# Kernel optimization log

Hardware: AMD Instinct MI355X
Metric: run time of the kernel (lower is better)

The kernel has to match this reference:

```python
import jax, jax.numpy as jnp
import numpy as np

N_HEADS = 16
D_EMBED = 1024


def setup_inputs() -> dict:
    key = jax.random.key(0)
    k_x, k_win, k_bin, k_wout, k_bout = jax.random.split(key, 5)
    B, S, D = 4, 2048, D_EMBED
    # weights stored as (in, out) so y = x @ W + b (equivalent to torch Linear)
    x = jax.random.normal(k_x, (B, S, D), dtype=jnp.float32)
    W_in = jax.random.normal(k_win, (D, 3 * D), dtype=jnp.float32) * (D ** -0.5)
    b_in = jax.random.normal(k_bin, (3 * D,), dtype=jnp.float32) * 0.02
    W_out = jax.random.normal(k_wout, (D, D), dtype=jnp.float32) * (D ** -0.5)
    b_out = jax.random.normal(k_bout, (D,), dtype=jnp.float32) * 0.02
    return {"x": x, "W_in": W_in, "b_in": b_in, "W_out": W_out, "b_out": b_out,
            "causal_mask": 1}


def reference(x, W_in, b_in, W_out, b_out, causal_mask):
    B, S, D = x.shape
    H = N_HEADS
    dh = D // H
    qkv = x @ W_in + b_in                      # [B,S,3D]
    q, k, v = jnp.split(qkv, 3, axis=-1)
    q = q.reshape(B, S, H, dh)
    k = k.reshape(B, S, H, dh)
    v = v.reshape(B, S, H, dh)
    scores = jnp.einsum('bqhd,bkhd->bhqk', q, k)   # [B,H,S,S]
    if causal_mask:
        # original masks with -inf BEFORE scaling; -inf/sqrt(dh) == -inf
        tri = jnp.triu(jnp.ones((S, S), dtype=bool), k=1)
        scores = jnp.where(tri, -jnp.inf, scores)
    scores = scores / jnp.sqrt(jnp.asarray(dh, dtype=scores.dtype))
    attn = jax.nn.softmax(scores, axis=-1)
    out = jnp.einsum('bhqk,bkhd->bqhd', attn, v).reshape(B, S, D)
    return out @ W_out + b_out
```

## Files before the change

kernel.cpp:

```cpp
#include <hip/hip_runtime.h>
#include <hip/hip_bf16.h>
#include <stdint.h>
#include <string.h>

#define S_LEN 2048
#define NH    16
#define DH    64
#define D_EMB 1024
#define CSCALE 0.18033688011112042f

typedef __attribute__((ext_vector_type(8)))  short short8;
typedef __attribute__((ext_vector_type(4)))  float f32x4;
typedef __attribute__((ext_vector_type(16))) float f32x16;

__device__ __forceinline__ unsigned short f2bf(float f) {
  uint32_t u = __builtin_bit_cast(uint32_t, f);
  uint32_t r = (u + 0x7FFFu + ((u >> 16) & 1u)) >> 16;
  return (unsigned short)r;
}

__device__ __forceinline__ uint32_t pkbf(float a, float b) {
  float2 f; f.x = a; f.y = b;
  __hip_bfloat162 h = __float22bfloat162_rn(f);
  uint32_t r;
  memcpy(&r, &h, 4);
  return r;
}

__device__ __forceinline__ void gload16(const void* g, void* l) {
  __builtin_amdgcn_global_load_lds(
      (__attribute__((address_space(1))) void*)(g),
      (__attribute__((address_space(3))) void*)(l),
      16, 0, 0);
}

__device__ __forceinline__ f32x16 mfma32(short8 a, short8 b, f32x16 c) {
  return __builtin_amdgcn_mfma_f32_32x32x16_bf16(a, b, c, 0, 0, 0);
}


__global__ __launch_bounds__(256)
void cvt_bf16(const float* __restrict__ in, unsigned short* __restrict__ out, int n) {
  int i = (blockIdx.x * 256 + threadIdx.x) * 4;
  if (i >= n) return;
  float4 v = *(const float4*)&in[i];
  ushort4 o;
  o.x = f2bf(v.x); o.y = f2bf(v.y); o.z = f2bf(v.z); o.w = f2bf(v.w);
  *(ushort4*)&out[i] = o;
}

__global__ __launch_bounds__(256)
void transpose_cvt(const float* __restrict__ in, unsigned short* __restrict__ out,
                   int R, int C) {
  __shared__ float t[64][65];
  const int nbr = R >> 6;
  const int br = (blockIdx.x % nbr) << 6;
  const int bc = (blockIdx.x / nbr) << 6;
  const int tid = threadIdx.x;
  const int tr = tid >> 4;
  const int tc = (tid & 15) << 2;
#pragma unroll
  for (int i = 0; i < 4; ++i) {
    float4 v = *(const float4*)&in[(size_t)(br + tr + i * 16) * C + bc + tc];
    t[tr + i * 16][tc + 0] = v.x;
    t[tr + i * 16][tc + 1] = v.y;
    t[tr + i * 16][tc + 2] = v.z;
    t[tr + i * 16][tc + 3] = v.w;
  }
  __syncthreads();
#pragma unroll
  for (int i = 0; i < 4; ++i) {
    int c = tr + i * 16;
    ushort4 o;
    o.x = f2bf(t[tc + 0][c]);
    o.y = f2bf(t[tc + 1][c]);
    o.z = f2bf(t[tc + 2][c]);
    o.w = f2bf(t[tc + 3][c]);
    *(ushort4*)&out[(size_t)(bc + c) * R + br + tc] = o;
  }
}


template <int MODE>
__global__ __launch_bounds__(256, 2)
void gemm_bt(const unsigned short* __restrict__ A,
             const unsigned short* __restrict__ Bt,
             const float* __restrict__ bias,
             unsigned short* __restrict__ q_out,
             unsigned short* __restrict__ k_out,
             unsigned short* __restrict__ v_out,
             float* __restrict__ f_out,
             int M, int N, int K) {
  __shared__ __attribute__((aligned(16))) unsigned short As[2][128 * 64];
  __shared__ __attribute__((aligned(16))) unsigned short Bs[2][128 * 64];
  const int tid  = threadIdx.x;
  const int lane = tid & 63;
  const int w    = tid >> 6;
  const int grp  = lane >> 4;
  const int lc   = lane & 15;
  const int nbn  = N >> 7;
  const int bm   = blockIdx.x / nbn;
  const int bn   = blockIdx.x % nbn;
  const int wr   = w >> 1, wc = w & 1;

  f32x4 acc[4][4];
#pragma unroll
  for (int m = 0; m < 4; ++m)
#pragma unroll
    for (int n = 0; n < 4; ++n) acc[m][n] = f32x4{0.f, 0.f, 0.f, 0.f};

  const int srow = lane >> 3;
  const int scol = ((lane & 7) ^ srow) * 8;
  const int nkt  = K >> 6;

#define GSTAGE(buf_, kt_) do {                                               \
    _Pragma("unroll")                                                        \
    for (int c_ = 0; c_ < 4; ++c_) {                                         \
      const int rc_ = w * 32 + c_ * 8;                                       \
      gload16(&A[(size_t)(bm * 128 + rc_ + srow) * K + (kt_) * 64 + scol],   \
              (void*)(&As[buf_][rc_ * 64]));                                 \
      gload16(&Bt[(size_t)(bn * 128 + rc_ + srow) * K + (kt_) * 64 + scol],  \
              (void*)(&Bs[buf_][rc_ * 64]));                                 \
    }                                                                        \
  } while (0)

  GSTAGE(0, 0);
  __syncthreads();

  for (int kt = 0; kt < nkt; ++kt) {
    const int cur = kt & 1;
    if (kt + 1 < nkt) GSTAGE(cur ^ 1, kt + 1);
#pragma unroll
    for (int kk = 0; kk < 2; ++kk) {
      short8 af[4], bf[4];
#pragma unroll
      for (int m = 0; m < 4; ++m) {
        const int row = wr * 64 + m * 16 + lc;
        const int cb  = ((kk * 4 + grp) ^ (lc & 7)) * 8;
        af[m] = *(const short8*)(&As[cur][row * 64 + cb]);
      }
#pragma unroll
      for (int n = 0; n < 4; ++n) {
        const int row = wc * 64 + n * 16 + lc;
        const int cb  = ((kk * 4 + grp) ^ (lc & 7)) * 8;
        bf[n] = *(const short8*)(&Bs[cur][row * 64 + cb]);
      }
      __builtin_amdgcn_s_setprio(1);
#pragma unroll
      for (int m = 0; m < 4; ++m)
#pragma unroll
        for (int n = 0; n < 4; ++n)
          acc[m][n] = __builtin_amdgcn_mfma_f32_16x16x32_bf16(af[m], bf[n], acc[m][n], 0, 0, 0);
      __builtin_amdgcn_s_setprio(0);
    }
    __syncthreads();
  }
#undef GSTAGE

  const int gm0 = bm * 128 + wr * 64;
  const int gn0 = bn * 128 + wc * 64;
  if (MODE == 0) {
    const int seg = gn0 >> 10;
#pragma unroll
    for (int m = 0; m < 4; ++m) {
#pragma unroll
      for (int n = 0; n < 4; ++n) {
        const int gn = gn0 + n * 16 + lc;
        const float bv = bias[gn];
        const int j = gn & 1023;
        const int h = j >> 6, d = j & 63;
        const int gmb = gm0 + m * 16 + grp * 4;
        const int b = gmb >> 11;
        const size_t bhb = ((size_t)(b * NH + h) * 32 + ((gmb & 2047) >> 6)) * 4096;
        if (seg == 2) {
          const size_t vi = bhb + ((d >> 5) * 4 + m) * 512 +
                            ((d & 31) + (grp >> 1) * 32) * 8 + (grp & 1) * 4;
          uint2 dv;
          dv.x = pkbf(acc[m][n][0] + bv, acc[m][n][1] + bv);
          dv.y = pkbf(acc[m][n][2] + bv, acc[m][n][3] + bv);
          *(uint2*)&v_out[vi] = dv;
        } else {
#pragma unroll
          for (int r = 0; r < 4; ++r) {
            const int s = (gmb + r) & 2047;
            float v = acc[m][n][r] + bv;
            if (seg == 0) v *= CSCALE;
            const size_t idx = bhb + (((s >> 5) & 1) * 4 + (d >> 4)) * 512 +
                               ((s & 31) + ((d >> 3) & 1) * 32) * 8 + (d & 7);
            if (seg == 0) q_out[idx] = f2bf(v); else k_out[idx] = f2bf(v);
          }
        }
      }
    }
  } else {
#pragma unroll
    for (int m = 0; m < 4; ++m) {
#pragma unroll
      for (int n = 0; n < 4; ++n) {
        const int gn = gn0 + n * 16 + lc;
        const float bv = bias[gn];
#pragma unroll
        for (int r = 0; r < 4; ++r) {
          const int gm = gm0 + m * 16 + grp * 4 + r;
          f_out[(size_t)gm * N + gn] = acc[m][n][r] + bv;
        }
      }
    }
  }
}


__global__ __launch_bounds__(256, 3)
void attn_fwd7(const unsigned short* __restrict__ Qp,
               const unsigned short* __restrict__ Kp,
               const unsigned short* __restrict__ Vp,
               unsigned short* __restrict__ Aout) {
  __shared__ __attribute__((aligned(16))) unsigned short Ks[2][4096];
  __shared__ __attribute__((aligned(16))) unsigned short Vs[2][4096];
  __shared__ __attribute__((aligned(16))) unsigned short Pl[4][32][64];
  const int tid  = threadIdx.x;
  const int lane = tid & 63, w = tid >> 6;
  const int q32  = lane & 31;
  const int hi   = lane >> 5;
  const int lof  = lane * 8;
  const int g    = blockIdx.x;
  const int t    = 15 - (g >> 6);
  const int bh   = (((g >> 3) & 7) << 3) | (g & 7);
  const int b    = bh >> 4, h = bh & 15;
  const size_t fb = (size_t)bh * 32;
  unsigned short* prow = &Pl[w][q32][0];
  const int swz = (q32 & 7) << 3;

#define STAGE(bf_, kb_) do {                                          \
    const size_t sb_ = (fb + (size_t)(kb_)) * 4096 + tid * 8;         \
    gload16(Kp + sb_,        (void*)&Ks[bf_][tid * 8]);               \
    gload16(Kp + sb_ + 2048, (void*)&Ks[bf_][2048 + tid * 8]);        \
    gload16(Vp + sb_,        (void*)&Vs[bf_][tid * 8]);               \
    gload16(Vp + sb_ + 2048, (void*)&Vs[bf_][2048 + tid * 8]);        \
  } while (0)

  const int qw0 = t * 128 + w * 32;
  const int qkb = 2 * t + (w >> 1), qsub = w & 1;

  short8 qf[4];
#pragma unroll
  for (int s = 0; s < 4; ++s)
    qf[s] = *(const short8*)(Qp + (fb + qkb) * 4096 + (qsub * 4 + s) * 512 + lof);

  f32x16 oa, ob;
#pragma unroll
  for (int rr = 0; rr < 16; ++rr) { oa[rr] = 0.f; ob[rr] = 0.f; }
  float l = 0.f;

  const int nbt = 2 * t + 2;
  STAGE(0, 0);
  asm volatile("s_waitcnt vmcnt(0)" ::: "memory");
  __syncthreads();
  int buf = 0;

#pragma unroll 1
  for (int kb = 0; kb < nbt; ++kb) {
    if (kb + 1 < nbt) STAGE(buf ^ 1, kb + 1);
    const int kvb = kb << 6;
    if (kvb <= qw0 + 31) {
      const unsigned short* kl = &Ks[buf][0];
      const unsigned short* vl = &Vs[buf][0];

      f32x16 c0, c1;
#pragma unroll
      for (int rr = 0; rr < 16; ++rr) { c0[rr] = 0.f; c1[rr] = -1e30f; }
#pragma unroll
      for (int s = 0; s < 4; ++s) {
        short8 kf = *(const short8*)(kl + s * 512 + lof);
        c0 = mfma32(kf, qf[s], c0);
      }
      const bool do1 = (kvb + 32 <= qw0 + 31);
      if (do1) {
#pragma unroll
        for (int rr = 0; rr < 16; ++rr) c1[rr] = 0.f;
#pragma unroll
        for (int s = 0; s < 4; ++s) {
          short8 kf = *(const short8*)(kl + (4 + s) * 512 + lof);
          c1 = mfma32(kf, qf[s], c1);
        }
      }

      if (kvb + 63 > qw0) {
        const int thr = qw0 + q32 - kvb;
#pragma unroll
        for (int rr = 0; rr < 16; ++rr) {
          const int k0 = (rr & 3) + 8 * (rr >> 2) + 4 * hi;
          if (k0 > thr)      c0[rr] = -1e30f;
          if (k0 + 32 > thr) c1[rr] = -1e30f;
        }
      }

#pragma unroll
      for (int rr = 0; rr < 16; ++rr) c0[rr] = exp2f(c0[rr]);
#pragma unroll
      for (int rr = 0; rr < 16; ++rr) c1[rr] = exp2f(c1[rr]);
      float tp[8];
#pragma unroll
      for (int i = 0; i < 8; ++i)
        tp[i] = (c0[i] + c0[i + 8]) + (c1[i] + c1[i + 8]);
      l += ((tp[0] + tp[1]) + (tp[2] + tp[3])) +
           ((tp[4] + tp[5]) + (tp[6] + tp[7]));

#pragma unroll
      for (int gg = 0; gg < 4; ++gg) {
        const int k0 = 8 * gg + 4 * hi;
        uint2 d0, d1;
        d0.x = pkbf(c0[4 * gg],     c0[4 * gg + 1]);
        d0.y = pkbf(c0[4 * gg + 2], c0[4 * gg + 3]);
        d1.x = pkbf(c1[4 * gg],     c1[4 * gg + 1]);
        d1.y = pkbf(c1[4 * gg + 2], c1[4 * gg + 3]);
        *(uint2*)&prow[k0 ^ swz]        = d0;
        *(uint2*)&prow[(k0 + 32) ^ swz] = d1;
      }
      asm volatile("s_waitcnt lgkmcnt(0)" ::: "memory");
      __builtin_amdgcn_sched_barrier(0);

      short8 bfr[4];
#pragma unroll
      for (int ks = 0; ks < 4; ++ks)
        bfr[ks] = *(const short8*)&prow[(ks * 16 + hi * 8) ^ swz];
#pragma unroll
      for (int ks = 0; ks < 2; ++ks) {
        oa = mfma32(*(const short8*)(vl + ks * 512 + lof), bfr[ks], oa);
        ob = mfma32(*(const short8*)(vl + (4 + ks) * 512 + lof), bfr[ks], ob);
      }
      if (do1) {
#pragma unroll
        for (int ks = 2; ks < 4; ++ks) {
          oa = mfma32(*(const short8*)(vl + ks * 512 + lof), bfr[ks], oa);
          ob = mfma32(*(const short8*)(vl + (4 + ks) * 512 + lof), bfr[ks], ob);
        }
      }
    }
    asm volatile("s_waitcnt vmcnt(0)" ::: "memory");
    __syncthreads();
    buf ^= 1;
  }

  l += __shfl_xor(l, 32);
  const float inv = 1.0f / l;
#pragma unroll
  for (int gg = 0; gg < 4; ++gg) {
    const int d0 = 8 * gg + 4 * hi;
    uint2 da, db;
    da.x = pkbf(oa[4 * gg] * inv,     oa[4 * gg + 1] * inv);
    da.y = pkbf(oa[4 * gg + 2] * inv, oa[4 * gg + 3] * inv);
    db.x = pkbf(ob[4 * gg] * inv,     ob[4 * gg + 1] * inv);
    db.y = pkbf(ob[4 * gg + 2] * inv, ob[4 * gg + 3] * inv);
    *(uint2*)&prow[d0 ^ swz]        = da;
    *(uint2*)&prow[(d0 + 32) ^ swz] = db;
  }
  asm volatile("s_waitcnt lgkmcnt(0)" ::: "memory");
  __builtin_amdgcn_sched_barrier(0);
  const int er = lane >> 1, eh = lane & 1;
  const int rswz = (er & 7) << 3;
  const unsigned short* lr = &Pl[w][er][0];
  unsigned short* op = Aout + ((size_t)(b * S_LEN + qw0 + er)) * D_EMB + h * DH + eh * 32;
#pragma unroll
  for (int jj = 0; jj < 4; ++jj) {
    short8 ov = *(const short8*)&lr[(eh * 32 + jj * 8) ^ rswz];
    *(short8*)(op + jj * 8) = ov;
  }
#undef STAGE
}


extern "C" void kernel_launch(void* const* d_in, const int* in_sizes, int n_in,
                              void* d_out, int out_size, void* d_ws, size_t ws_size,
                              hipStream_t stream) {
  const float* x     = (const float*)d_in[0];
  const float* W_in  = (const float*)d_in[1];
  const float* b_in  = (const float*)d_in[2];
  const float* W_out = (const float*)d_in[3];
  const float* b_out = (const float*)d_in[4];

  char* ws = (char*)d_ws;
  unsigned short* xb  = (unsigned short*)(ws);
  unsigned short* Wti = (unsigned short*)(ws + 16777216);
  unsigned short* Wto = (unsigned short*)(ws + 23068672);
  unsigned short* Qb  = (unsigned short*)(ws + 25165824);
  unsigned short* Kb  = (unsigned short*)(ws + 41943040);
  unsigned short* Vb  = (unsigned short*)(ws + 58720256);
  float* out = (float*)d_out;

  cvt_bf16<<<8192, 256, 0, stream>>>(x, xb, 8388608);
  transpose_cvt<<<16 * 48, 256, 0, stream>>>(W_in, Wti, 1024, 3072);
  transpose_cvt<<<16 * 16, 256, 0, stream>>>(W_out, Wto, 1024, 1024);

  gemm_bt<0><<<64 * 24, 256, 0, stream>>>(xb, Wti, b_in, Qb, Kb, Vb, nullptr,
                                          8192, 3072, 1024);
  attn_fwd7<<<1024, 256, 0, stream>>>(Qb, Kb, Vb, xb);
  gemm_bt<1><<<64 * 8, 256, 0, stream>>>(xb, Wto, b_out, nullptr, nullptr, nullptr, out,
                                         8192, 1024, 1024);
}
```

Before: 186.8 us.

## Pass softmax probabilities to PV MFMA via permlane32 swap instead of LDS

Result: no change. 185.1 us (-0.9%).

```diff
diff --git a/kernel.cpp b/kernel.cpp
--- a/kernel.cpp
+++ b/kernel.cpp
@@ -12,6 +12,7 @@
 typedef __attribute__((ext_vector_type(8)))  short short8;
 typedef __attribute__((ext_vector_type(4)))  float f32x4;
 typedef __attribute__((ext_vector_type(16))) float f32x16;
+typedef __attribute__((ext_vector_type(4)))  uint32_t u32x4;
 
 __device__ __forceinline__ unsigned short f2bf(float f) {
   uint32_t u = __builtin_bit_cast(uint32_t, f);
@@ -211,13 +212,12 @@
 
 
 __global__ __launch_bounds__(256, 3)
-void attn_fwd7(const unsigned short* __restrict__ Qp,
+void attn_fwd8(const unsigned short* __restrict__ Qp,
                const unsigned short* __restrict__ Kp,
                const unsigned short* __restrict__ Vp,
                unsigned short* __restrict__ Aout) {
   __shared__ __attribute__((aligned(16))) unsigned short Ks[2][4096];
   __shared__ __attribute__((aligned(16))) unsigned short Vs[2][4096];
-  __shared__ __attribute__((aligned(16))) unsigned short Pl[4][32][64];
   const int tid  = threadIdx.x;
   const int lane = tid & 63, w = tid >> 6;
   const int q32  = lane & 31;
@@ -228,8 +228,6 @@
   const int bh   = (((g >> 3) & 7) << 3) | (g & 7);
   const int b    = bh >> 4, h = bh & 15;
   const size_t fb = (size_t)bh * 32;
-  unsigned short* prow = &Pl[w][q32][0];
-  const int swz = (q32 & 7) << 3;
 
 #define STAGE(bf_, kb_) do {                                          \
     const size_t sb_ = (fb + (size_t)(kb_)) * 4096 + tid * 8;         \
@@ -269,12 +267,13 @@
       f32x16 c0, c1;
 #pragma unroll
       for (int rr = 0; rr < 16; ++rr) { c0[rr] = 0.f; c1[rr] = -1e30f; }
+      const bool do1 = (kvb + 32 <= qw0 + 31);
+      __builtin_amdgcn_s_setprio(1);
 #pragma unroll
       for (int s = 0; s < 4; ++s) {
         short8 kf = *(const short8*)(kl + s * 512 + lof);
         c0 = mfma32(kf, qf[s], c0);
       }
-      const bool do1 = (kvb + 32 <= qw0 + 31);
       if (do1) {
 #pragma unroll
         for (int rr = 0; rr < 16; ++rr) c1[rr] = 0.f;
@@ -284,6 +283,7 @@
           c1 = mfma32(kf, qf[s], c1);
         }
       }
+      __builtin_amdgcn_s_setprio(0);
 
       if (kvb + 63 > qw0) {
         const int thr = qw0 + q32 - kvb;
@@ -307,34 +307,28 @@
            ((tp[4] + tp[5]) + (tp[6] + tp[7]));
 
 #pragma unroll
-      for (int gg = 0; gg < 4; ++gg) {
-        const int k0 = 8 * gg + 4 * hi;
-        uint2 d0, d1;
-        d0.x = pkbf(c0[4 * gg],     c0[4 * gg + 1]);
-        d0.y = pkbf(c0[4 * gg + 2], c0[4 * gg + 3]);
-        d1.x = pkbf(c1[4 * gg],     c1[4 * gg + 1]);
-        d1.y = pkbf(c1[4 * gg + 2], c1[4 * gg + 3]);
-        *(uint2*)&prow[k0 ^ swz]        = d0;
-        *(uint2*)&prow[(k0 + 32) ^ swz] = d1;
-      }
-      asm volatile("s_waitcnt lgkmcnt(0)" ::: "memory");
-      __builtin_amdgcn_sched_barrier(0);
-
-      short8 bfr[4];
-#pragma unroll
-      for (int ks = 0; ks < 4; ++ks)
-        bfr[ks] = *(const short8*)&prow[(ks * 16 + hi * 8) ^ swz];
-#pragma unroll
-      for (int ks = 0; ks < 2; ++ks) {
-        oa = mfma32(*(const short8*)(vl + ks * 512 + lof), bfr[ks], oa);
-        ob = mfma32(*(const short8*)(vl + (4 + ks) * 512 + lof), bfr[ks], ob);
-      }
-      if (do1) {
-#pragma unroll
-        for (int ks = 2; ks < 4; ++ks) {
-          oa = mfma32(*(const short8*)(vl + ks * 512 + lof), bfr[ks], oa);
-          ob = mfma32(*(const short8*)(vl + (4 + ks) * 512 + lof), bfr[ks], ob);
-        }
+      for (int ks = 0; ks < 4; ++ks) {
+        if (ks >= 2 && !do1) break;
+        uint32_t pA, pB, pC, pD;
+        if (ks == 0) {
+          pA = pkbf(c0[0],  c0[1]);  pB = pkbf(c0[2],  c0[3]);
+          pC = pkbf(c0[4],  c0[5]);  pD = pkbf(c0[6],  c0[7]);
+        } else if (ks == 1) {
+          pA = pkbf(c0[8],  c0[9]);  pB = pkbf(c0[10], c0[11]);
+          pC = pkbf(c0[12], c0[13]); pD = pkbf(c0[14], c0[15]);
+        } else if (ks == 2) {
+          pA = pkbf(c1[0],  c1[1]);  pB = pkbf(c1[2],  c1[3]);
+          pC = pkbf(c1[4],  c1[5]);  pD = pkbf(c1[6],  c1[7]);
+        } else {
+          pA = pkbf(c1[8],  c1[9]);  pB = pkbf(c1[10], c1[11]);
+          pC = pkbf(c1[12], c1[13]); pD = pkbf(c1[14], c1[15]);
+        }
+        auto r0 = __builtin_amdgcn_permlane32_swap(pA, pC, false, false);
+        auto r1 = __builtin_amdgcn_permlane32_swap(pB, pD, false, false);
+        u32x4 fw; fw[0] = r0[0]; fw[1] = r1[0]; fw[2] = r0[1]; fw[3] = r1[1];
+        const short8 frag = __builtin_bit_cast(short8, fw);
+        oa = mfma32(*(const short8*)(vl + ks * 512 + lof), frag, oa);
+        ob = mfma32(*(const short8*)(vl + (4 + ks) * 512 + lof), frag, ob);
       }
     }
     asm volatile("s_waitcnt vmcnt(0)" ::: "memory");
@@ -344,6 +338,9 @@
 
   l += __shfl_xor(l, 32);
   const float inv = 1.0f / l;
+  unsigned short* ebuf = (unsigned short*)Ks;
+  unsigned short* prow = ebuf + (w * 32 + q32) * 64;
+  const int swz = (q32 & 7) << 3;
 #pragma unroll
   for (int gg = 0; gg < 4; ++gg) {
     const int d0 = 8 * gg + 4 * hi;
@@ -359,7 +356,7 @@
   __builtin_amdgcn_sched_barrier(0);
   const int er = lane >> 1, eh = lane & 1;
   const int rswz = (er & 7) << 3;
-  const unsigned short* lr = &Pl[w][er][0];
+  const unsigned short* lr = ebuf + (w * 32 + er) * 64;
   unsigned short* op = Aout + ((size_t)(b * S_LEN + qw0 + er)) * D_EMB + h * DH + eh * 32;
 #pragma unroll
   for (int jj = 0; jj < 4; ++jj) {
@@ -394,7 +391,7 @@
 
   gemm_bt<0><<<64 * 24, 256, 0, stream>>>(xb, Wti, b_in, Qb, Kb, Vb, nullptr,
                                           8192, 3072, 1024);
-  attn_fwd7<<<1024, 256, 0, stream>>>(Qb, Kb, Vb, xb);
+  attn_fwd8<<<1024, 256, 0, stream>>>(Qb, Kb, Vb, xb);
   gemm_bt<1><<<64 * 8, 256, 0, stream>>>(xb, Wto, b_out, nullptr, nullptr, nullptr, out,
                                          8192, 1024, 1024);
 }
```
